# Performance work log

Measured on AMD Instinct MI355X. Metric: run time of the kernel, lower is better.

## Reference

```python
import jax, jax.numpy as jnp
import numpy as np

B = 512          # batch of visual features
VF_D = 4096      # visual feature dim (VGG fc7)
HID_D = 2048     # hidden dim
EMB_D = 300      # order-embedding / label-vector dim
N_LABELS = 2000  # number of GT label vectors


def setup_inputs() -> dict:
    key = jax.random.key(0)
    ks = jax.random.split(key, 4)
    vfs = jax.random.normal(ks[0], (B, VF_D), dtype=jnp.float32)
    W1 = jax.random.normal(ks[1], (VF_D, HID_D), dtype=jnp.float32) * (1.0 / np.sqrt(VF_D))
    b1 = jnp.zeros((HID_D,), dtype=jnp.float32)
    W2 = jax.random.normal(ks[2], (HID_D, EMB_D), dtype=jnp.float32) * (1.0 / np.sqrt(HID_D))
    b2 = jnp.zeros((EMB_D,), dtype=jnp.float32)
    gt_label_vecs = jax.random.normal(ks[3], (N_LABELS, EMB_D), dtype=jnp.float32)
    return {"vfs": vfs, "W1": W1, "b1": b1, "W2": W2, "b2": b2,
            "gt_label_vecs": gt_label_vecs}


def reference(vfs, W1, b1, W2, b2, gt_label_vecs):
    # hidden_layer: ReLU -> (Dropout, identity at eval) -> Linear
    vf_hidden = jnp.dot(jax.nn.relu(vfs), W1) + b1            # [B, HID_D]
    # embedding_layer: ReLU -> Linear
    vf_emb = jnp.dot(jax.nn.relu(vf_hidden), W2) + b2         # [B, EMB_D]
    # order_sim(hypers=gt_label_vecs, hypos=vf_emb):
    #   score = -|| clamp(hypo - hyper, min=0) ||^2, batched over all pairs
    diff = jax.nn.relu(vf_emb[:, None, :] - gt_label_vecs[None, :, :])  # [B, N, D]
    score_stack = -jnp.sum(diff * diff, axis=-1)              # [B, N_LABELS]
    return score_stack, vf_emb
```

## Files before the change

kernel.cpp:

```cpp
#include <hip/hip_runtime.h>

#define B_SZ   512
#define VFD    4096
#define HIDD   2048
#define EMBD   300
#define NLAB   2000
#define NPAD   320

#define G1_SPLIT 4
#define G2_SPLIT 8
#define SD_SPLIT 4

typedef __attribute__((ext_vector_type(8))) short short8x;
typedef __attribute__((ext_vector_type(4))) float f32x4;
typedef __attribute__((ext_vector_type(8))) unsigned short ushort8;
typedef __attribute__((ext_vector_type(4))) unsigned short ushort4x;

typedef const __attribute__((address_space(1))) unsigned int* gas_t;
typedef __attribute__((address_space(3))) unsigned int* las_t;

__device__ inline unsigned short f2bf(float x) {
    unsigned u = __float_as_uint(x);
    u += 0x7FFF + ((u >> 16) & 1);
    return (unsigned short)(u >> 16);
}

__global__ __launch_bounds__(256) void prep_kernel(
    const float* __restrict__ vfs, unsigned short* __restrict__ Xb,
    const float* __restrict__ W1, unsigned short* __restrict__ W1T,
    const float* __restrict__ W2, unsigned short* __restrict__ W2T,
    float* __restrict__ scores)
{
    __shared__ unsigned int Lds[64][34];
    const int tid = threadIdx.x;
    const int blk = blockIdx.x;

    if (blk < 1024) {
        const int i = (blk * 256 + tid) * 8;
        float4 a = *(const float4*)&vfs[i];
        float4 b = *(const float4*)&vfs[i + 4];
        ushort8 o;
        o[0] = f2bf(fmaxf(a.x, 0.f)); o[1] = f2bf(fmaxf(a.y, 0.f));
        o[2] = f2bf(fmaxf(a.z, 0.f)); o[3] = f2bf(fmaxf(a.w, 0.f));
        o[4] = f2bf(fmaxf(b.x, 0.f)); o[5] = f2bf(fmaxf(b.y, 0.f));
        o[6] = f2bf(fmaxf(b.z, 0.f)); o[7] = f2bf(fmaxf(b.w, 0.f));
        *(ushort8*)&Xb[i] = o;
        return;
    }
    if (blk >= 3232) {
        const int i = ((blk - 3232) * 256 + tid) * 4;
        if (i < B_SZ * NLAB) {
            float4 z = {0.f, 0.f, 0.f, 0.f};
            *(float4*)&scores[i] = z;
        }
        return;
    }

    const float* in; unsigned short* out; int N, ldK, bx, by;
    if (blk < 3072) {
        const int b = blk - 1024;
        in = W1; out = W1T; N = HIDD; ldK = VFD; bx = b & 31; by = b >> 5;
    } else {
        const int b = blk - 3072;
        in = W2; out = W2T; N = EMBD; ldK = HIDD; bx = b % 5; by = b / 5;
    }
    const int n0 = bx * 64, k0 = by * 64;

    #pragma unroll
    for (int i = 0; i < 2; ++i) {
        const int s = tid + 256 * i;
        const int kp = s >> 4, nq = s & 15;
        const int n = n0 + nq * 4;
        float4 v0 = {0.f,0.f,0.f,0.f}, v1 = {0.f,0.f,0.f,0.f};
        if (n < N) {
            v0 = *(const float4*)&in[(size_t)(k0 + 2 * kp)     * N + n];
            v1 = *(const float4*)&in[(size_t)(k0 + 2 * kp + 1) * N + n];
        }
        Lds[nq*4+0][kp] = (unsigned)f2bf(v0.x) | ((unsigned)f2bf(v1.x) << 16);
        Lds[nq*4+1][kp] = (unsigned)f2bf(v0.y) | ((unsigned)f2bf(v1.y) << 16);
        Lds[nq*4+2][kp] = (unsigned)f2bf(v0.z) | ((unsigned)f2bf(v1.z) << 16);
        Lds[nq*4+3][kp] = (unsigned)f2bf(v0.w) | ((unsigned)f2bf(v1.w) << 16);
    }
    __syncthreads();

    #pragma unroll
    for (int i = 0; i < 2; ++i) {
        const int c = tid + 256 * i;
        const int n = c >> 3, oct = c & 7;
        uint2 lo = *(uint2*)&Lds[n][oct * 4];
        uint2 hi = *(uint2*)&Lds[n][oct * 4 + 2];
        uint4 v = make_uint4(lo.x, lo.y, hi.x, hi.y);
        *(uint4*)&out[(size_t)(n0 + n) * ldK + k0 + oct * 8] = v;
    }
}

__global__ __launch_bounds__(256) void gemm1_kernel(
    const unsigned short* __restrict__ A,
    const unsigned short* __restrict__ Bt,
    float* __restrict__ Cpart)
{
    __shared__ unsigned short As[2][4096];
    __shared__ unsigned short Bs[2][8192];

    const int tid = threadIdx.x;
    const int m0 = blockIdx.y * 64, n0 = blockIdx.x * 128;
    const int kbase = blockIdx.z * (VFD / G1_SPLIT);

    const unsigned short* ga = A + (size_t)(m0 + (tid & 63)) * VFD + kbase + (tid >> 6) * 8;
    const unsigned short* gb = Bt + (size_t)(n0 + (tid & 127)) * VFD + kbase + (tid >> 7) * 8;

    const int lane = tid & 63;
    const int wave = tid >> 6;
    const int wm = (wave & 1) * 32;
    const int wn = (wave >> 1) * 64;
    const int q = lane >> 4, l15 = lane & 15;

    f32x4 acc[2][4];
    #pragma unroll
    for (int r = 0; r < 2; ++r)
        #pragma unroll
        for (int c = 0; c < 4; ++c) acc[r][c] = (f32x4){0.f,0.f,0.f,0.f};

    #pragma unroll
    for (int i = 0; i < 2; ++i)
        __builtin_amdgcn_global_load_lds((gas_t)(const void*)(ga + i * 32),
                                         (las_t)(void*)&As[0][(tid + 256 * i) * 8], 16, 0, 0);
    #pragma unroll
    for (int i = 0; i < 4; ++i)
        __builtin_amdgcn_global_load_lds((gas_t)(const void*)(gb + i * 16),
                                         (las_t)(void*)&Bs[0][(tid + 256 * i) * 8], 16, 0, 0);

    const int iters = (VFD / G1_SPLIT) / 64;
    for (int t = 0; t < iters; ++t) {
        const int cur = t & 1, nxt = cur ^ 1;
        __syncthreads();

        if (t + 1 < iters) {
            const int ko = (t + 1) * 64;
            #pragma unroll
            for (int i = 0; i < 2; ++i)
                __builtin_amdgcn_global_load_lds((gas_t)(const void*)(ga + ko + i * 32),
                                                 (las_t)(void*)&As[nxt][(tid + 256 * i) * 8], 16, 0, 0);
            #pragma unroll
            for (int i = 0; i < 4; ++i)
                __builtin_amdgcn_global_load_lds((gas_t)(const void*)(gb + ko + i * 16),
                                                 (las_t)(void*)&Bs[nxt][(tid + 256 * i) * 8], 16, 0, 0);
        }

        #pragma unroll
        for (int kk = 0; kk < 2; ++kk) {
            const int oct = kk * 4 + q;
            short8x a0 = *(short8x*)&As[cur][(oct * 64 + wm +      l15) * 8];
            short8x a1 = *(short8x*)&As[cur][(oct * 64 + wm + 16 + l15) * 8];
            #pragma unroll
            for (int c = 0; c < 4; ++c) {
                short8x b = *(short8x*)&Bs[cur][(oct * 128 + wn + c * 16 + l15) * 8];
                acc[0][c] = __builtin_amdgcn_mfma_f32_16x16x32_bf16(a0, b, acc[0][c], 0, 0, 0);
                acc[1][c] = __builtin_amdgcn_mfma_f32_16x16x32_bf16(a1, b, acc[1][c], 0, 0, 0);
            }
        }
    }

    float* Cz = Cpart + (size_t)blockIdx.z * B_SZ * HIDD;
    #pragma unroll
    for (int r = 0; r < 2; ++r) {
        #pragma unroll
        for (int g = 0; g < 4; ++g) {
            const int rr = m0 + wm + r * 16 + q * 4 + g;
            #pragma unroll
            for (int c = 0; c < 4; ++c)
                Cz[(size_t)rr * HIDD + n0 + wn + c * 16 + l15] = acc[r][c][g];
        }
    }
}

template<int LDA, int LDB, int LDC, int KCHUNK>
__global__ __launch_bounds__(256) void gemm_bf16_kernel(
    const unsigned short* __restrict__ A,
    const unsigned short* __restrict__ Bt,
    float* __restrict__ Cpart, int M)
{
    __shared__ unsigned short As[2][4096];
    __shared__ unsigned short Bs[2][4096];

    const int tid = threadIdx.x;
    const int m0 = blockIdx.y * 64, n0 = blockIdx.x * 64;
    const int kbase = blockIdx.z * KCHUNK;

    const unsigned short* ga = A  + (size_t)(m0 + (tid & 63)) * LDA + kbase + (tid >> 6) * 8;
    const unsigned short* gb = Bt + (size_t)(n0 + (tid & 63)) * LDB + kbase + (tid >> 6) * 8;

    const int lane = tid & 63;
    const int wave = tid >> 6;
    const int wm = (wave & 1) * 32;
    const int wn = (wave >> 1) * 32;
    const int q = lane >> 4, l15 = lane & 15;

    f32x4 acc00 = {0.f,0.f,0.f,0.f}, acc01 = {0.f,0.f,0.f,0.f};
    f32x4 acc10 = {0.f,0.f,0.f,0.f}, acc11 = {0.f,0.f,0.f,0.f};

    #pragma unroll
    for (int i = 0; i < 2; ++i) {
        __builtin_amdgcn_global_load_lds((gas_t)(const void*)(ga + i * 32),
                                         (las_t)(void*)&As[0][(tid + 256 * i) * 8], 16, 0, 0);
        __builtin_amdgcn_global_load_lds((gas_t)(const void*)(gb + i * 32),
                                         (las_t)(void*)&Bs[0][(tid + 256 * i) * 8], 16, 0, 0);
    }

    const int iters = KCHUNK / 64;
    for (int t = 0; t < iters; ++t) {
        const int cur = t & 1, nxt = cur ^ 1;
        __syncthreads();

        if (t + 1 < iters) {
            const int ko = (t + 1) * 64;
            #pragma unroll
            for (int i = 0; i < 2; ++i) {
                __builtin_amdgcn_global_load_lds((gas_t)(const void*)(ga + ko + i * 32),
                                                 (las_t)(void*)&As[nxt][(tid + 256 * i) * 8], 16, 0, 0);
                __builtin_amdgcn_global_load_lds((gas_t)(const void*)(gb + ko + i * 32),
                                                 (las_t)(void*)&Bs[nxt][(tid + 256 * i) * 8], 16, 0, 0);
            }
        }

        #pragma unroll
        for (int kk = 0; kk < 2; ++kk) {
            const int oct = kk * 4 + q;
            short8x a0 = *(short8x*)&As[cur][(oct * 64 + wm +      l15) * 8];
            short8x a1 = *(short8x*)&As[cur][(oct * 64 + wm + 16 + l15) * 8];
            short8x b0 = *(short8x*)&Bs[cur][(oct * 64 + wn +      l15) * 8];
            short8x b1 = *(short8x*)&Bs[cur][(oct * 64 + wn + 16 + l15) * 8];
            acc00 = __builtin_amdgcn_mfma_f32_16x16x32_bf16(a0, b0, acc00, 0, 0, 0);
            acc01 = __builtin_amdgcn_mfma_f32_16x16x32_bf16(a0, b1, acc01, 0, 0, 0);
            acc10 = __builtin_amdgcn_mfma_f32_16x16x32_bf16(a1, b0, acc10, 0, 0, 0);
            acc11 = __builtin_amdgcn_mfma_f32_16x16x32_bf16(a1, b1, acc11, 0, 0, 0);
        }
    }

    float* Cz = Cpart + (size_t)blockIdx.z * M * LDC;
    #pragma unroll
    for (int r = 0; r < 4; ++r) {
        const int rr = m0 + wm + q * 4 + r;
        const int cc = n0 + wn + l15;
        Cz[(size_t)rr * LDC + cc]             = acc00[r];
        Cz[(size_t)rr * LDC + cc + 16]        = acc01[r];
        Cz[(size_t)(rr + 16) * LDC + cc]      = acc10[r];
        Cz[(size_t)(rr + 16) * LDC + cc + 16] = acc11[r];
    }
}

__global__ __launch_bounds__(256) void reduce_h_kernel(
    const float* __restrict__ Hpart, const float* __restrict__ b1,
    unsigned short* __restrict__ Hb)
{
    const int i = (blockIdx.x * 256 + threadIdx.x) * 4;
    const int col = i & (HIDD - 1);
    float4 s = *(const float4*)&b1[col];
    #pragma unroll
    for (int z = 0; z < G1_SPLIT; ++z) {
        float4 p = *(const float4*)&Hpart[(size_t)z * B_SZ * HIDD + i];
        s.x += p.x; s.y += p.y; s.z += p.z; s.w += p.w;
    }
    ushort4x o;
    o[0] = f2bf(fmaxf(s.x, 0.f));
    o[1] = f2bf(fmaxf(s.y, 0.f));
    o[2] = f2bf(fmaxf(s.z, 0.f));
    o[3] = f2bf(fmaxf(s.w, 0.f));
    *(ushort4x*)&Hb[i] = o;
}

__global__ __launch_bounds__(256) void reduce_e_kernel(
    const float* __restrict__ Epart, const float* __restrict__ b2,
    float* __restrict__ E)
{
    const int gid = blockIdx.x * 256 + threadIdx.x;
    if (gid >= B_SZ * EMBD) return;
    const int m = gid / EMBD, n = gid - m * EMBD;
    float v = b2[n];
    #pragma unroll
    for (int z = 0; z < G2_SPLIT; ++z)
        v += Epart[(size_t)z * B_SZ * NPAD + m * NPAD + n];
    E[gid] = v;
}

__global__ __launch_bounds__(128) void scores_part_kernel(
    const float* __restrict__ E, const float* __restrict__ G,
    float* __restrict__ scores)
{
    __shared__ float Gs[64][44];

    const int tid = threadIdx.x;
    const int tx = tid & 15, ty = tid >> 4;
    const int n0 = blockIdx.x * 64, b0 = blockIdx.y * 32;
    const int dbase = blockIdx.z * (NPAD / SD_SPLIT);

    float acc[4][4] = {};

    for (int dc = 0; dc < NPAD / SD_SPLIT; dc += 40) {
        const int d0 = dbase + dc;
        __syncthreads();
        #pragma unroll
        for (int i = 0; i < 5; ++i) {
            const int s = tid + 128 * i;
            const int row = s / 10, qd = (s - row * 10) * 4;
            const int d = d0 + qd;
            const int n = n0 + row;
            float4 v = {0.f, 0.f, 0.f, 0.f};
            if (n < NLAB && d < EMBD) v = *(const float4*)&G[(size_t)n * EMBD + d];
            *(float4*)&Gs[row][qd] = v;
        }
        __syncthreads();

        #pragma unroll 2
        for (int d = 0; d < 40; d += 4) {
            const int dd = d0 + d;
            float4 e[4];
            if (dd < EMBD) {
                #pragma unroll
                for (int r = 0; r < 4; ++r)
                    e[r] = *(const float4*)&E[(size_t)(b0 + ty * 4 + r) * EMBD + dd];
            } else {
                #pragma unroll
                for (int r = 0; r < 4; ++r) e[r] = make_float4(0.f, 0.f, 0.f, 0.f);
            }
            #pragma unroll
            for (int c = 0; c < 4; ++c) {
                float4 g = *(float4*)&Gs[tx + 16 * c][d];
                #pragma unroll
                for (int r = 0; r < 4; ++r) {
                    float t;
                    t = fmaxf(e[r].x - g.x, 0.f); acc[r][c] += t * t;
                    t = fmaxf(e[r].y - g.y, 0.f); acc[r][c] += t * t;
                    t = fmaxf(e[r].z - g.z, 0.f); acc[r][c] += t * t;
                    t = fmaxf(e[r].w - g.w, 0.f); acc[r][c] += t * t;
                }
            }
        }
    }

    #pragma unroll
    for (int r = 0; r < 4; ++r) {
        const int b = b0 + ty * 4 + r;
        #pragma unroll
        for (int c = 0; c < 4; ++c) {
            const int n = n0 + tx + 16 * c;
            if (n < NLAB) atomicAdd(&scores[(size_t)b * NLAB + n], -acc[r][c]);
        }
    }
}

extern "C" void kernel_launch(void* const* d_in, const int* in_sizes, int n_in,
                              void* d_out, int out_size, void* d_ws, size_t ws_size,
                              hipStream_t stream)
{
    const float* vfs = (const float*)d_in[0];
    const float* W1  = (const float*)d_in[1];
    const float* b1  = (const float*)d_in[2];
    const float* W2  = (const float*)d_in[3];
    const float* b2  = (const float*)d_in[4];
    const float* G   = (const float*)d_in[5];

    float* out    = (float*)d_out;
    float* scores = out;
    float* E      = out + (size_t)B_SZ * NLAB;

    char* ws = (char*)d_ws;
    unsigned short* Xb  = (unsigned short*)(ws);
    unsigned short* W1T = (unsigned short*)(ws + 4194304);
    unsigned short* W2T = (unsigned short*)(ws + 20971520);
    unsigned short* Hb  = (unsigned short*)(ws + 22282240);
    float*          Hpart = (float*)(ws + 24379392);
    float*          Epart = (float*)(ws + 41156608);

    prep_kernel<<<4256, 256, 0, stream>>>(vfs, Xb, W1, W1T, W2, W2T, scores);

    gemm1_kernel<<<dim3(16, 8, G1_SPLIT), 256, 0, stream>>>(Xb, W1T, Hpart);
    reduce_h_kernel<<<1024, 256, 0, stream>>>(Hpart, b1, Hb);

    gemm_bf16_kernel<HIDD, HIDD, NPAD, HIDD / G2_SPLIT>
        <<<dim3(5, 8, G2_SPLIT), 256, 0, stream>>>(Hb, W2T, Epart, B_SZ);
    reduce_e_kernel<<<600, 256, 0, stream>>>(Epart, b2, E);

    scores_part_kernel<<<dim3(32, 16, SD_SPLIT), 128, 0, stream>>>(E, G, scores);
}
```

Baseline: 170.2 us.

## Fuse GEMM, reduction and score stages into one cooperative persistent kernel

Replaces the five-kernel chain after prep with a single cooperative kernel of 512 blocks that runs GEMM1, the hidden-layer reduction with bias and ReLU, GEMM2, and the order-similarity scores, separated by grid-wide syncs. GEMM2 now accumulates straight into E with atomics after E is pre-filled with the bias, which removes the separate Epart reduction. The score stage pulls tiles from an atomic work counter. This is meant to remove launch gaps and intermediate passes, but it adds grid.sync costs, atomic contention and float-atomic ordering nondeterminism, and depends on cooperative launch succeeding, with the old kernels as a fallback.

```diff
diff --git a/kernel.cpp b/kernel.cpp
--- a/kernel.cpp
+++ b/kernel.cpp
@@ -1,4 +1,7 @@
 #include <hip/hip_runtime.h>
+#include <hip/hip_cooperative_groups.h>
+
+namespace cg = cooperative_groups;
 
 #define B_SZ   512
 #define VFD    4096
@@ -94,6 +97,274 @@
     }
 }
 
+__global__ __launch_bounds__(256, 2) void mega_kernel(
+    const unsigned short* __restrict__ Xb,
+    const unsigned short* __restrict__ W1T,
+    float* __restrict__ Hpart,
+    const float* __restrict__ b1,
+    unsigned short* __restrict__ Hb,
+    const unsigned short* __restrict__ W2T,
+    const float* __restrict__ b2,
+    float* __restrict__ E,
+    const float* __restrict__ G,
+    float* __restrict__ scores,
+    unsigned int* __restrict__ counter)
+{
+    __shared__ __align__(16) unsigned char smem[49152];
+    __shared__ int sVb;
+
+    cg::grid_group grid = cg::this_grid();
+    const int tid = threadIdx.x;
+    const int blk = blockIdx.x;
+    const int lane = tid & 63;
+    const int wave = tid >> 6;
+    const int q = lane >> 4, l15 = lane & 15;
+
+    {
+        unsigned short (*As)[4096] = (unsigned short(*)[4096])smem;
+        unsigned short (*Bs)[8192] = (unsigned short(*)[8192])(smem + 16384);
+
+        const int bx = blk & 15, by = (blk >> 4) & 7, bz = blk >> 7;
+        const int m0 = by * 64, n0 = bx * 128;
+        const int kbase = bz * (VFD / G1_SPLIT);
+
+        const unsigned short* ga = Xb  + (size_t)(m0 + (tid & 63)) * VFD + kbase + (tid >> 6) * 8;
+        const unsigned short* gb = W1T + (size_t)(n0 + (tid & 127)) * VFD + kbase + (tid >> 7) * 8;
+
+        const int wm = (wave & 1) * 32;
+        const int wn = (wave >> 1) * 64;
+
+        f32x4 acc[2][4];
+        #pragma unroll
+        for (int r = 0; r < 2; ++r)
+            #pragma unroll
+            for (int c = 0; c < 4; ++c) acc[r][c] = (f32x4){0.f,0.f,0.f,0.f};
+
+        #pragma unroll
+        for (int i = 0; i < 2; ++i)
+            __builtin_amdgcn_global_load_lds((gas_t)(const void*)(ga + i * 32),
+                                             (las_t)(void*)&As[0][(tid + 256 * i) * 8], 16, 0, 0);
+        #pragma unroll
+        for (int i = 0; i < 4; ++i)
+            __builtin_amdgcn_global_load_lds((gas_t)(const void*)(gb + i * 16),
+                                             (las_t)(void*)&Bs[0][(tid + 256 * i) * 8], 16, 0, 0);
+
+        const int iters = (VFD / G1_SPLIT) / 64;
+        for (int t = 0; t < iters; ++t) {
+            const int cur = t & 1, nxt = cur ^ 1;
+            __syncthreads();
+
+            if (t + 1 < iters) {
+                const int ko = (t + 1) * 64;
+                #pragma unroll
+                for (int i = 0; i < 2; ++i)
+                    __builtin_amdgcn_global_load_lds((gas_t)(const void*)(ga + ko + i * 32),
+                                                     (las_t)(void*)&As[nxt][(tid + 256 * i) * 8], 16, 0, 0);
+                #pragma unroll
+                for (int i = 0; i < 4; ++i)
+                    __builtin_amdgcn_global_load_lds((gas_t)(const void*)(gb + ko + i * 16),
+                                                     (las_t)(void*)&Bs[nxt][(tid + 256 * i) * 8], 16, 0, 0);
+            }
+
+            #pragma unroll
+            for (int kk = 0; kk < 2; ++kk) {
+                const int oct = kk * 4 + q;
+                short8x a0 = *(short8x*)&As[cur][(oct * 64 + wm +      l15) * 8];
+                short8x a1 = *(short8x*)&As[cur][(oct * 64 + wm + 16 + l15) * 8];
+                #pragma unroll
+                for (int c = 0; c < 4; ++c) {
+                    short8x b = *(short8x*)&Bs[cur][(oct * 128 + wn + c * 16 + l15) * 8];
+                    acc[0][c] = __builtin_amdgcn_mfma_f32_16x16x32_bf16(a0, b, acc[0][c], 0, 0, 0);
+                    acc[1][c] = __builtin_amdgcn_mfma_f32_16x16x32_bf16(a1, b, acc[1][c], 0, 0, 0);
+                }
+            }
+        }
+
+        float* Cz = Hpart + (size_t)bz * B_SZ * HIDD;
+        #pragma unroll
+        for (int r = 0; r < 2; ++r)
+            #pragma unroll
+            for (int g = 0; g < 4; ++g) {
+                const int rr = m0 + wm + r * 16 + q * 4 + g;
+                #pragma unroll
+                for (int c = 0; c < 4; ++c)
+                    Cz[(size_t)rr * HIDD + n0 + wn + c * 16 + l15] = acc[r][c][g];
+            }
+    }
+
+    __threadfence();
+    grid.sync();
+
+    for (int v = blk; v < 1175; v += 512) {
+        if (v < 1024) {
+            const int i = (v * 256 + tid) * 4;
+            const int col = i & (HIDD - 1);
+            float4 s = *(const float4*)&b1[col];
+            #pragma unroll
+            for (int z = 0; z < G1_SPLIT; ++z) {
+                float4 p = *(const float4*)&Hpart[(size_t)z * B_SZ * HIDD + i];
+                s.x += p.x; s.y += p.y; s.z += p.z; s.w += p.w;
+            }
+            ushort4x o;
+            o[0] = f2bf(fmaxf(s.x, 0.f));
+            o[1] = f2bf(fmaxf(s.y, 0.f));
+            o[2] = f2bf(fmaxf(s.z, 0.f));
+            o[3] = f2bf(fmaxf(s.w, 0.f));
+            *(ushort4x*)&Hb[i] = o;
+        } else if (v < 1174) {
+            const int j = ((v - 1024) * 256 + tid) * 4;
+            const int n = j % 300;
+            *(float4*)&E[j] = *(const float4*)&b2[n];
+        } else if (tid == 0) {
+            *counter = 0u;
+        }
+    }
+
+    __threadfence();
+    grid.sync();
+
+    if (blk < 320) {
+        unsigned short (*As2)[4096] = (unsigned short(*)[4096])smem;
+        unsigned short (*Bs2)[4096] = (unsigned short(*)[4096])(smem + 16384);
+
+        const int bx = blk % 5, by = (blk / 5) & 7, bz = blk / 40;
+        const int m0 = by * 64, n0 = bx * 64;
+        const int kbase = bz * (HIDD / G2_SPLIT);
+
+        const unsigned short* ga = Hb  + (size_t)(m0 + (tid & 63)) * HIDD + kbase + (tid >> 6) * 8;
+        const unsigned short* gb = W2T + (size_t)(n0 + (tid & 63)) * HIDD + kbase + (tid >> 6) * 8;
+
+        const int wm = (wave & 1) * 32;
+        const int wn = (wave >> 1) * 32;
+
+        f32x4 acc00 = {0.f,0.f,0.f,0.f}, acc01 = {0.f,0.f,0.f,0.f};
+        f32x4 acc10 = {0.f,0.f,0.f,0.f}, acc11 = {0.f,0.f,0.f,0.f};
+
+        #pragma unroll
+        for (int i = 0; i < 2; ++i) {
+            __builtin_amdgcn_global_load_lds((gas_t)(const void*)(ga + i * 32),
+                                             (las_t)(void*)&As2[0][(tid + 256 * i) * 8], 16, 0, 0);
+            __builtin_amdgcn_global_load_lds((gas_t)(const void*)(gb + i * 32),
+                                             (las_t)(void*)&Bs2[0][(tid + 256 * i) * 8], 16, 0, 0);
+        }
+
+        const int iters = (HIDD / G2_SPLIT) / 64;
+        for (int t = 0; t < iters; ++t) {
+            const int cur = t & 1, nxt = cur ^ 1;
+            __syncthreads();
+
+            if (t + 1 < iters) {
+                const int ko = (t + 1) * 64;
+                #pragma unroll
+                for (int i = 0; i < 2; ++i) {
+                    __builtin_amdgcn_global_load_lds((gas_t)(const void*)(ga + ko + i * 32),
+                                                     (las_t)(void*)&As2[nxt][(tid + 256 * i) * 8], 16, 0, 0);
+                    __builtin_amdgcn_global_load_lds((gas_t)(const void*)(gb + ko + i * 32),
+                                                     (las_t)(void*)&Bs2[nxt][(tid + 256 * i) * 8], 16, 0, 0);
+                }
+            }
+
+            #pragma unroll
+            for (int kk = 0; kk < 2; ++kk) {
+                const int oct = kk * 4 + q;
+                short8x a0 = *(short8x*)&As2[cur][(oct * 64 + wm +      l15) * 8];
+                short8x a1 = *(short8x*)&As2[cur][(oct * 64 + wm + 16 + l15) * 8];
+                short8x b0 = *(short8x*)&Bs2[cur][(oct * 64 + wn +      l15) * 8];
+                short8x b1 = *(short8x*)&Bs2[cur][(oct * 64 + wn + 16 + l15) * 8];
+                acc00 = __builtin_amdgcn_mfma_f32_16x16x32_bf16(a0, b0, acc00, 0, 0, 0);
+                acc01 = __builtin_amdgcn_mfma_f32_16x16x32_bf16(a0, b1, acc01, 0, 0, 0);
+                acc10 = __builtin_amdgcn_mfma_f32_16x16x32_bf16(a1, b0, acc10, 0, 0, 0);
+                acc11 = __builtin_amdgcn_mfma_f32_16x16x32_bf16(a1, b1, acc11, 0, 0, 0);
+            }
+        }
+
+        const int cc = n0 + wn + l15;
+        #pragma unroll
+        for (int r = 0; r < 4; ++r) {
+            const int rr = m0 + wm + q * 4 + r;
+            if (cc < EMBD)      atomicAdd(&E[(size_t)rr * EMBD + cc],        acc00[r]);
+            if (cc + 16 < EMBD) atomicAdd(&E[(size_t)rr * EMBD + cc + 16],   acc01[r]);
+            if (cc < EMBD)      atomicAdd(&E[(size_t)(rr + 16) * EMBD + cc], acc10[r]);
+            if (cc + 16 < EMBD) atomicAdd(&E[(size_t)(rr + 16) * EMBD + cc + 16], acc11[r]);
+        }
+    }
+
+    __threadfence();
+    grid.sync();
+
+    {
+        float (*Gs)[44] = (float(*)[44])smem;
+        const int tx = tid & 15, ty4 = (tid >> 4) * 4;
+
+        for (;;) {
+            if (tid == 0) sVb = (int)atomicAdd(counter, 1u);
+            __syncthreads();
+            const int v = sVb;
+            if (v >= 1024) break;
+
+            const int n0 = (v & 31) * 64;
+            const int b0 = ((v >> 5) & 7) * 64;
+            const int dbase = (v >> 8) * 80;
+
+            float acc[4][4] = {};
+
+            for (int dc = 0; dc < 80; dc += 40) {
+                const int d0 = dbase + dc;
+                __syncthreads();
+                #pragma unroll
+                for (int i = 0; i < 3; ++i) {
+                    const int s = tid + 256 * i;
+                    if (s < 640) {
+                        const int row = s / 10, qd = (s - row * 10) * 4;
+                        const int d = d0 + qd;
+                        const int n = n0 + row;
+                        float4 vv = {0.f, 0.f, 0.f, 0.f};
+                        if (n < NLAB && d < EMBD) vv = *(const float4*)&G[(size_t)n * EMBD + d];
+                        *(float4*)&Gs[row][qd] = vv;
+                    }
+                }
+                __syncthreads();
+
+                #pragma unroll 2
+                for (int d = 0; d < 40; d += 4) {
+                    const int dd = d0 + d;
+                    float4 e[4];
+                    if (dd < EMBD) {
+                        #pragma unroll
+                        for (int r = 0; r < 4; ++r)
+                            e[r] = *(const float4*)&E[(size_t)(b0 + ty4 + r) * EMBD + dd];
+                    } else {
+                        #pragma unroll
+                        for (int r = 0; r < 4; ++r) e[r] = make_float4(0.f, 0.f, 0.f, 0.f);
+                    }
+                    #pragma unroll
+                    for (int c = 0; c < 4; ++c) {
+                        float4 g = *(float4*)&Gs[tx + 16 * c][d];
+                        #pragma unroll
+                        for (int r = 0; r < 4; ++r) {
+                            float t;
+                            t = fmaxf(e[r].x - g.x, 0.f); acc[r][c] += t * t;
+                            t = fmaxf(e[r].y - g.y, 0.f); acc[r][c] += t * t;
+                            t = fmaxf(e[r].z - g.z, 0.f); acc[r][c] += t * t;
+                            t = fmaxf(e[r].w - g.w, 0.f); acc[r][c] += t * t;
+                        }
+                    }
+                }
+            }
+
+            #pragma unroll
+            for (int r = 0; r < 4; ++r) {
+                const int b = b0 + ty4 + r;
+                #pragma unroll
+                for (int c = 0; c < 4; ++c) {
+                    const int n = n0 + tx + 16 * c;
+                    if (n < NLAB) atomicAdd(&scores[(size_t)b * NLAB + n], -acc[r][c]);
+                }
+            }
+        }
+    }
+}
+
 __global__ __launch_bounds__(256) void gemm1_kernel(
     const unsigned short* __restrict__ A,
     const unsigned short* __restrict__ Bt,
@@ -163,7 +434,7 @@
 
     float* Cz = Cpart + (size_t)blockIdx.z * B_SZ * HIDD;
     #pragma unroll
-    for (int r = 0; r < 2; ++r) {
+    for (int r = 0; r < 2; ++r)
         #pragma unroll
         for (int g = 0; g < 4; ++g) {
             const int rr = m0 + wm + r * 16 + q * 4 + g;
@@ -171,7 +442,6 @@
             for (int c = 0; c < 4; ++c)
                 Cz[(size_t)rr * HIDD + n0 + wn + c * 16 + l15] = acc[r][c][g];
         }
-    }
 }
 
 template<int LDA, int LDB, int LDC, int KCHUNK>
@@ -371,15 +641,26 @@
     unsigned short* Hb  = (unsigned short*)(ws + 22282240);
     float*          Hpart = (float*)(ws + 24379392);
     float*          Epart = (float*)(ws + 41156608);
+    unsigned int*   counter = (unsigned int*)(ws + 47185920);
 
     prep_kernel<<<4256, 256, 0, stream>>>(vfs, Xb, W1, W1T, W2, W2T, scores);
 
-    gemm1_kernel<<<dim3(16, 8, G1_SPLIT), 256, 0, stream>>>(Xb, W1T, Hpart);
-    reduce_h_kernel<<<1024, 256, 0, stream>>>(Hpart, b1, Hb);
-
-    gemm_bf16_kernel<HIDD, HIDD, NPAD, HIDD / G2_SPLIT>
-        <<<dim3(5, 8, G2_SPLIT), 256, 0, stream>>>(Hb, W2T, Epart, B_SZ);
-    reduce_e_kernel<<<600, 256, 0, stream>>>(Epart, b2, E);
-
-    scores_part_kernel<<<dim3(32, 16, SD_SPLIT), 128, 0, stream>>>(E, G, scores);
-}
+    const unsigned short* Xb_c  = Xb;
+    const unsigned short* W1T_c = W1T;
+    const unsigned short* W2T_c = W2T;
+    void* kargs[] = {
+        (void*)&Xb_c, (void*)&W1T_c, (void*)&Hpart, (void*)&b1, (void*)&Hb,
+        (void*)&W2T_c, (void*)&b2, (void*)&E, (void*)&G, (void*)&scores,
+        (void*)&counter
+    };
+    hipError_t cerr = hipLaunchCooperativeKernel((void*)mega_kernel, dim3(512),
+                                                 dim3(256), kargs, 0, stream);
+    if (cerr != hipSuccess) {
+        gemm1_kernel<<<dim3(16, 8, G1_SPLIT), 256, 0, stream>>>(Xb, W1T, Hpart);
+        reduce_h_kernel<<<1024, 256, 0, stream>>>(Hpart, b1, Hb);
+        gemm_bf16_kernel<HIDD, HIDD, NPAD, HIDD / G2_SPLIT>
+            <<<dim3(5, 8, G2_SPLIT), 256, 0, stream>>>(Hb, W2T, Epart, B_SZ);
+        reduce_e_kernel<<<600, 256, 0, stream>>>(Epart, b2, E);
+        scores_part_kernel<<<dim3(32, 16, SD_SPLIT), 128, 0, stream>>>(E, G, scores);
+    }
+}
```

Result: slower. 514.3 us (+202.2%).

## Drop split-K partial buffers: fuse bias/ReLU into GEMM1, atomic-accumulate GEMM2

Applied to the files above, without the earlier changes.

GEMM1 no longer uses split-K. It runs 256 blocks of 64x64 tiles over the full K and applies bias, ReLU and bf16 conversion in its epilogue, which removes the Hpart buffer and the reduce_h kernel. GEMM2 keeps split-K but accumulates with atomicAdd directly into E, which the prep kernel pre-initialises with b2. This removes the Epart buffer and the reduce_e kernel. The cost is a longer serial K loop per block with fewer blocks in GEMM1, plus atomic contention and non-deterministic summation order in GEMM2.

```diff
diff --git a/kernel.cpp b/kernel.cpp
--- a/kernel.cpp
+++ b/kernel.cpp
@@ -7,14 +7,12 @@
 #define NLAB   2000
 #define NPAD   320
 
-#define G1_SPLIT 4
 #define G2_SPLIT 8
 #define SD_SPLIT 4
 
 typedef __attribute__((ext_vector_type(8))) short short8x;
 typedef __attribute__((ext_vector_type(4))) float f32x4;
 typedef __attribute__((ext_vector_type(8))) unsigned short ushort8;
-typedef __attribute__((ext_vector_type(4))) unsigned short ushort4x;
 
 typedef const __attribute__((address_space(1))) unsigned int* gas_t;
 typedef __attribute__((address_space(3))) unsigned int* las_t;
@@ -29,7 +27,8 @@
     const float* __restrict__ vfs, unsigned short* __restrict__ Xb,
     const float* __restrict__ W1, unsigned short* __restrict__ W1T,
     const float* __restrict__ W2, unsigned short* __restrict__ W2T,
-    float* __restrict__ scores)
+    float* __restrict__ scores, const float* __restrict__ b2,
+    float* __restrict__ E)
 {
     __shared__ unsigned int Lds[64][34];
     const int tid = threadIdx.x;
@@ -47,6 +46,14 @@
         *(ushort8*)&Xb[i] = o;
         return;
     }
+    if (blk >= 4232) {
+        const int j = ((blk - 4232) * 256 + tid) * 4;
+        if (j < B_SZ * EMBD) {
+            const int n = j % EMBD;
+            *(float4*)&E[j] = *(const float4*)&b2[n];
+        }
+        return;
+    }
     if (blk >= 3232) {
         const int i = ((blk - 3232) * 256 + tid) * 4;
         if (i < B_SZ * NLAB) {
@@ -97,98 +104,17 @@
 __global__ __launch_bounds__(256) void gemm1_kernel(
     const unsigned short* __restrict__ A,
     const unsigned short* __restrict__ Bt,
-    float* __restrict__ Cpart)
-{
-    __shared__ unsigned short As[2][4096];
-    __shared__ unsigned short Bs[2][8192];
-
-    const int tid = threadIdx.x;
-    const int m0 = blockIdx.y * 64, n0 = blockIdx.x * 128;
-    const int kbase = blockIdx.z * (VFD / G1_SPLIT);
-
-    const unsigned short* ga = A + (size_t)(m0 + (tid & 63)) * VFD + kbase + (tid >> 6) * 8;
-    const unsigned short* gb = Bt + (size_t)(n0 + (tid & 127)) * VFD + kbase + (tid >> 7) * 8;
-
-    const int lane = tid & 63;
-    const int wave = tid >> 6;
-    const int wm = (wave & 1) * 32;
-    const int wn = (wave >> 1) * 64;
-    const int q = lane >> 4, l15 = lane & 15;
-
-    f32x4 acc[2][4];
-    #pragma unroll
-    for (int r = 0; r < 2; ++r)
-        #pragma unroll
-        for (int c = 0; c < 4; ++c) acc[r][c] = (f32x4){0.f,0.f,0.f,0.f};
-
-    #pragma unroll
-    for (int i = 0; i < 2; ++i)
-        __builtin_amdgcn_global_load_lds((gas_t)(const void*)(ga + i * 32),
-                                         (las_t)(void*)&As[0][(tid + 256 * i) * 8], 16, 0, 0);
-    #pragma unroll
-    for (int i = 0; i < 4; ++i)
-        __builtin_amdgcn_global_load_lds((gas_t)(const void*)(gb + i * 16),
-                                         (las_t)(void*)&Bs[0][(tid + 256 * i) * 8], 16, 0, 0);
-
-    const int iters = (VFD / G1_SPLIT) / 64;
-    for (int t = 0; t < iters; ++t) {
-        const int cur = t & 1, nxt = cur ^ 1;
-        __syncthreads();
-
-        if (t + 1 < iters) {
-            const int ko = (t + 1) * 64;
-            #pragma unroll
-            for (int i = 0; i < 2; ++i)
-                __builtin_amdgcn_global_load_lds((gas_t)(const void*)(ga + ko + i * 32),
-                                                 (las_t)(void*)&As[nxt][(tid + 256 * i) * 8], 16, 0, 0);
-            #pragma unroll
-            for (int i = 0; i < 4; ++i)
-                __builtin_amdgcn_global_load_lds((gas_t)(const void*)(gb + ko + i * 16),
-                                                 (las_t)(void*)&Bs[nxt][(tid + 256 * i) * 8], 16, 0, 0);
-        }
-
-        #pragma unroll
-        for (int kk = 0; kk < 2; ++kk) {
-            const int oct = kk * 4 + q;
-            short8x a0 = *(short8x*)&As[cur][(oct * 64 + wm +      l15) * 8];
-            short8x a1 = *(short8x*)&As[cur][(oct * 64 + wm + 16 + l15) * 8];
-            #pragma unroll
-            for (int c = 0; c < 4; ++c) {
-                short8x b = *(short8x*)&Bs[cur][(oct * 128 + wn + c * 16 + l15) * 8];
-                acc[0][c] = __builtin_amdgcn_mfma_f32_16x16x32_bf16(a0, b, acc[0][c], 0, 0, 0);
-                acc[1][c] = __builtin_amdgcn_mfma_f32_16x16x32_bf16(a1, b, acc[1][c], 0, 0, 0);
-            }
-        }
-    }
-
-    float* Cz = Cpart + (size_t)blockIdx.z * B_SZ * HIDD;
-    #pragma unroll
-    for (int r = 0; r < 2; ++r) {
-        #pragma unroll
-        for (int g = 0; g < 4; ++g) {
-            const int rr = m0 + wm + r * 16 + q * 4 + g;
-            #pragma unroll
-            for (int c = 0; c < 4; ++c)
-                Cz[(size_t)rr * HIDD + n0 + wn + c * 16 + l15] = acc[r][c][g];
-        }
-    }
-}
-
-template<int LDA, int LDB, int LDC, int KCHUNK>
-__global__ __launch_bounds__(256) void gemm_bf16_kernel(
-    const unsigned short* __restrict__ A,
-    const unsigned short* __restrict__ Bt,
-    float* __restrict__ Cpart, int M)
+    const float* __restrict__ b1,
+    unsigned short* __restrict__ Hb)
 {
     __shared__ unsigned short As[2][4096];
     __shared__ unsigned short Bs[2][4096];
 
     const int tid = threadIdx.x;
     const int m0 = blockIdx.y * 64, n0 = blockIdx.x * 64;
-    const int kbase = blockIdx.z * KCHUNK;
-
-    const unsigned short* ga = A  + (size_t)(m0 + (tid & 63)) * LDA + kbase + (tid >> 6) * 8;
-    const unsigned short* gb = Bt + (size_t)(n0 + (tid & 63)) * LDB + kbase + (tid >> 6) * 8;
+
+    const unsigned short* ga = A  + (size_t)(m0 + (tid & 63)) * VFD + (tid >> 6) * 8;
+    const unsigned short* gb = Bt + (size_t)(n0 + (tid & 63)) * VFD + (tid >> 6) * 8;
 
     const int lane = tid & 63;
     const int wave = tid >> 6;
@@ -207,7 +133,7 @@
                                          (las_t)(void*)&Bs[0][(tid + 256 * i) * 8], 16, 0, 0);
     }
 
-    const int iters = KCHUNK / 64;
+    const int iters = VFD / 64;
     for (int t = 0; t < iters; ++t) {
         const int cur = t & 1, nxt = cur ^ 1;
         __syncthreads();
@@ -237,50 +163,89 @@
         }
     }
 
-    float* Cz = Cpart + (size_t)blockIdx.z * M * LDC;
+    const int cc = n0 + wn + l15;
+    const float bL = b1[cc], bH = b1[cc + 16];
     #pragma unroll
     for (int r = 0; r < 4; ++r) {
         const int rr = m0 + wm + q * 4 + r;
-        const int cc = n0 + wn + l15;
-        Cz[(size_t)rr * LDC + cc]             = acc00[r];
-        Cz[(size_t)rr * LDC + cc + 16]        = acc01[r];
-        Cz[(size_t)(rr + 16) * LDC + cc]      = acc10[r];
-        Cz[(size_t)(rr + 16) * LDC + cc + 16] = acc11[r];
-    }
-}
-
-__global__ __launch_bounds__(256) void reduce_h_kernel(
-    const float* __restrict__ Hpart, const float* __restrict__ b1,
-    unsigned short* __restrict__ Hb)
-{
-    const int i = (blockIdx.x * 256 + threadIdx.x) * 4;
-    const int col = i & (HIDD - 1);
-    float4 s = *(const float4*)&b1[col];
-    #pragma unroll
-    for (int z = 0; z < G1_SPLIT; ++z) {
-        float4 p = *(const float4*)&Hpart[(size_t)z * B_SZ * HIDD + i];
-        s.x += p.x; s.y += p.y; s.z += p.z; s.w += p.w;
-    }
-    ushort4x o;
-    o[0] = f2bf(fmaxf(s.x, 0.f));
-    o[1] = f2bf(fmaxf(s.y, 0.f));
-    o[2] = f2bf(fmaxf(s.z, 0.f));
-    o[3] = f2bf(fmaxf(s.w, 0.f));
-    *(ushort4x*)&Hb[i] = o;
-}
-
-__global__ __launch_bounds__(256) void reduce_e_kernel(
-    const float* __restrict__ Epart, const float* __restrict__ b2,
+        Hb[(size_t)rr * HIDD + cc]             = f2bf(fmaxf(acc00[r] + bL, 0.f));
+        Hb[(size_t)rr * HIDD + cc + 16]        = f2bf(fmaxf(acc01[r] + bH, 0.f));
+        Hb[(size_t)(rr + 16) * HIDD + cc]      = f2bf(fmaxf(acc10[r] + bL, 0.f));
+        Hb[(size_t)(rr + 16) * HIDD + cc + 16] = f2bf(fmaxf(acc11[r] + bH, 0.f));
+    }
+}
+
+__global__ __launch_bounds__(256) void gemm2_kernel(
+    const unsigned short* __restrict__ A,
+    const unsigned short* __restrict__ Bt,
     float* __restrict__ E)
 {
-    const int gid = blockIdx.x * 256 + threadIdx.x;
-    if (gid >= B_SZ * EMBD) return;
-    const int m = gid / EMBD, n = gid - m * EMBD;
-    float v = b2[n];
-    #pragma unroll
-    for (int z = 0; z < G2_SPLIT; ++z)
-        v += Epart[(size_t)z * B_SZ * NPAD + m * NPAD + n];
-    E[gid] = v;
+    __shared__ unsigned short As[2][4096];
+    __shared__ unsigned short Bs[2][4096];
+
+    const int tid = threadIdx.x;
+    const int m0 = blockIdx.y * 64, n0 = blockIdx.x * 64;
+    const int kbase = blockIdx.z * (HIDD / G2_SPLIT);
+
+    const unsigned short* ga = A  + (size_t)(m0 + (tid & 63)) * HIDD + kbase + (tid >> 6) * 8;
+    const unsigned short* gb = Bt + (size_t)(n0 + (tid & 63)) * HIDD + kbase + (tid >> 6) * 8;
+
+    const int lane = tid & 63;
+    const int wave = tid >> 6;
+    const int wm = (wave & 1) * 32;
+    const int wn = (wave >> 1) * 32;
+    const int q = lane >> 4, l15 = lane & 15;
+
+    f32x4 acc00 = {0.f,0.f,0.f,0.f}, acc01 = {0.f,0.f,0.f,0.f};
+    f32x4 acc10 = {0.f,0.f,0.f,0.f}, acc11 = {0.f,0.f,0.f,0.f};
+
+    #pragma unroll
+    for (int i = 0; i < 2; ++i) {
+        __builtin_amdgcn_global_load_lds((gas_t)(const void*)(ga + i * 32),
+                                         (las_t)(void*)&As[0][(tid + 256 * i) * 8], 16, 0, 0);
+        __builtin_amdgcn_global_load_lds((gas_t)(const void*)(gb + i * 32),
+                                         (las_t)(void*)&Bs[0][(tid + 256 * i) * 8], 16, 0, 0);
+    }
+
+    const int iters = (HIDD / G2_SPLIT) / 64;
+    for (int t = 0; t < iters; ++t) {
+        const int cur = t & 1, nxt = cur ^ 1;
+        __syncthreads();
+
+        if (t + 1 < iters) {
+            const int ko = (t + 1) * 64;
+            #pragma unroll
+            for (int i = 0; i < 2; ++i) {
+                __builtin_amdgcn_global_load_lds((gas_t)(const void*)(ga + ko + i * 32),
+                                                 (las_t)(void*)&As[nxt][(tid + 256 * i) * 8], 16, 0, 0);
+                __builtin_amdgcn_global_load_lds((gas_t)(const void*)(gb + ko + i * 32),
+                                                 (las_t)(void*)&Bs[nxt][(tid + 256 * i) * 8], 16, 0, 0);
+            }
+        }
+
+        #pragma unroll
+        for (int kk = 0; kk < 2; ++kk) {
+            const int oct = kk * 4 + q;
+            short8x a0 = *(short8x*)&As[cur][(oct * 64 + wm +      l15) * 8];
+            short8x a1 = *(short8x*)&As[cur][(oct * 64 + wm + 16 + l15) * 8];
+            short8x b0 = *(short8x*)&Bs[cur][(oct * 64 + wn +      l15) * 8];
+            short8x b1 = *(short8x*)&Bs[cur][(oct * 64 + wn + 16 + l15) * 8];
+            acc00 = __builtin_amdgcn_mfma_f32_16x16x32_bf16(a0, b0, acc00, 0, 0, 0);
+            acc01 = __builtin_amdgcn_mfma_f32_16x16x32_bf16(a0, b1, acc01, 0, 0, 0);
+            acc10 = __builtin_amdgcn_mfma_f32_16x16x32_bf16(a1, b0, acc10, 0, 0, 0);
+            acc11 = __builtin_amdgcn_mfma_f32_16x16x32_bf16(a1, b1, acc11, 0, 0, 0);
+        }
+    }
+
+    const int cc = n0 + wn + l15;
+    #pragma unroll
+    for (int r = 0; r < 4; ++r) {
+        const int rr = m0 + wm + q * 4 + r;
+        if (cc < EMBD)      atomicAdd(&E[(size_t)rr * EMBD + cc],        acc00[r]);
+        if (cc + 16 < EMBD) atomicAdd(&E[(size_t)rr * EMBD + cc + 16],   acc01[r]);
+        if (cc < EMBD)      atomicAdd(&E[(size_t)(rr + 16) * EMBD + cc], acc10[r]);
+        if (cc + 16 < EMBD) atomicAdd(&E[(size_t)(rr + 16) * EMBD + cc + 16], acc11[r]);
+    }
 }
 
 __global__ __launch_bounds__(128) void scores_part_kernel(
@@ -369,17 +334,13 @@
     unsigned short* W1T = (unsigned short*)(ws + 4194304);
     unsigned short* W2T = (unsigned short*)(ws + 20971520);
     unsigned short* Hb  = (unsigned short*)(ws + 22282240);
-    float*          Hpart = (float*)(ws + 24379392);
-    float*          Epart = (float*)(ws + 41156608);
-
-    prep_kernel<<<4256, 256, 0, stream>>>(vfs, Xb, W1, W1T, W2, W2T, scores);
-
-    gemm1_kernel<<<dim3(16, 8, G1_SPLIT), 256, 0, stream>>>(Xb, W1T, Hpart);
-    reduce_h_kernel<<<1024, 256, 0, stream>>>(Hpart, b1, Hb);
-
-    gemm_bf16_kernel<HIDD, HIDD, NPAD, HIDD / G2_SPLIT>
-        <<<dim3(5, 8, G2_SPLIT), 256, 0, stream>>>(Hb, W2T, Epart, B_SZ);
-    reduce_e_kernel<<<600, 256, 0, stream>>>(Epart, b2, E);
+
+    prep_kernel<<<4382, 256, 0, stream>>>(vfs, Xb, W1, W1T, W2, W2T,
+                                          scores, b2, E);
+
+    gemm1_kernel<<<dim3(32, 8), 256, 0, stream>>>(Xb, W1T, b1, Hb);
+
+    gemm2_kernel<<<dim3(5, 8, G2_SPLIT), 256, 0, stream>>>(Hb, W2T, E);
 
     scores_part_kernel<<<dim3(32, 16, SD_SPLIT), 128, 0, stream>>>(E, G, scores);
 }
```

New measurement: 195.0 us. 1.15x slower.
